# Kernel tuning notes

Hardware: AMD Instinct MI355X
Metric: run time of the kernel (lower is better)

The kernel has to match this reference:

```python
import jax, jax.numpy as jnp
import numpy as np

HEAD_DIM = 64
N_HEADS = 64
N_KV = 8
Q_MULT = N_HEADS // N_KV  # 8
HIDDEN = 2880
SEQ = 1024
BATCH = 2
SLIDING_WINDOW = 128  # layer_idx=0 -> window active
ROPE_THETA = 150000.0
SCALING = 32.0
NTK_ALPHA = 1.0
NTK_BETA = 32.0
INIT_CTX = 4096
EPS = 1e-5


def _rope_caches(seq_len):
    # YaRN rotary caches (static numpy precompute, as in the source module)
    steps = np.arange(0, HEAD_DIM, 2, dtype=np.float32)
    freq = np.power(np.float32(ROPE_THETA), steps / np.float32(HEAD_DIM))
    concentration = np.float32(0.1) * np.log(np.float32(SCALING)) + 1.0
    d_half = np.float32(HEAD_DIM / 2.0)
    log_base = np.log(np.float32(ROPE_THETA))
    low = d_half * np.log(np.float32(INIT_CTX) / (np.float32(NTK_BETA) * np.float32(2.0 * np.pi))) / log_base
    high = d_half * np.log(np.float32(INIT_CTX) / (np.float32(NTK_ALPHA) * np.float32(2.0 * np.pi))) / log_base
    ramp = (np.arange(HEAD_DIM // 2, dtype=np.float32) - low) / (high - low)
    mask = 1.0 - np.clip(ramp, 0.0, 1.0)
    inv_freq = (1.0 / (np.float32(SCALING) * freq)) * (1.0 - mask) + (1.0 / freq) * mask
    pos = np.arange(seq_len, dtype=np.float32)
    freqs = np.einsum('i,j->ij', pos, inv_freq.astype(np.float32))
    cos = (np.cos(freqs) * concentration).astype(np.float32)
    sin = (np.sin(freqs) * concentration).astype(np.float32)
    return jnp.asarray(cos), jnp.asarray(sin)


def _apply_rotary(t, cos, sin):
    # t: (B, S, ..., head_dim); cos/sin: (S, head_dim//2). Rotate-half style.
    shape = (1, t.shape[1]) + (1,) * (t.ndim - 3) + (cos.shape[-1],)
    c = cos.reshape(shape)
    s = sin.reshape(shape)
    first, second = jnp.split(t, 2, axis=-1)
    return jnp.concatenate([first * c - second * s, second * c + first * s], axis=-1)


def setup_inputs() -> dict:
    key = jax.random.key(0)
    ks = jax.random.split(key, 6)
    qkv_dim = (N_HEADS + 2 * N_KV) * HEAD_DIM  # 5120
    return {
        'x': jax.random.normal(ks[0], (BATCH, SEQ, HIDDEN), dtype=jnp.float32),
        'norm_w': jnp.ones((HIDDEN,), dtype=jnp.float32),
        'qkv_w': jax.random.normal(ks[1], (qkv_dim, HIDDEN), dtype=jnp.float32) * 0.02,
        'qkv_b': jax.random.normal(ks[2], (qkv_dim,), dtype=jnp.float32) * 0.02,
        'out_w': jax.random.normal(ks[3], (HIDDEN, N_HEADS * HEAD_DIM), dtype=jnp.float32) * 0.02,
        'out_b': jax.random.normal(ks[4], (HIDDEN,), dtype=jnp.float32) * 0.02,
        'sinks': jax.random.normal(ks[5], (N_HEADS,), dtype=jnp.float32),
    }


def reference(x, norm_w, qkv_w, qkv_b, out_w, out_b, sinks):
    B, S, _ = x.shape
    # RMSNorm (fp32 accumulation)
    xf = x.astype(jnp.float32)
    rms = jnp.mean(xf * xf, axis=-1, keepdims=True)
    t = (xf * jax.lax.rsqrt(rms + EPS) * norm_w).astype(x.dtype)
    # QKV projection (fp32 accumulation)
    qkv = jnp.matmul(t.astype(jnp.float32), qkv_w.T) + qkv_b
    q_dim = N_HEADS * HEAD_DIM
    kv_dim = N_KV * HEAD_DIM
    q = qkv[..., :q_dim].reshape(B, S, N_KV, Q_MULT, HEAD_DIM)
    k = qkv[..., q_dim:q_dim + kv_dim].reshape(B, S, N_KV, HEAD_DIM)
    v = qkv[..., q_dim + kv_dim:].reshape(B, S, N_KV, HEAD_DIM)
    # YaRN rotary embedding
    cos, sin = _rope_caches(S)
    q = _apply_rotary(q, cos, sin)
    k = _apply_rotary(k, cos, sin)
    # causal + sliding-window mask
    neg_inf = jnp.float32(-jnp.inf)
    mask = jnp.triu(jnp.full((S, S), neg_inf, dtype=jnp.float32), k=1)
    mask = mask + jnp.tril(jnp.full((S, S), neg_inf, dtype=jnp.float32), k=-SLIDING_WINDOW)
    sm_scale = jnp.float32(1.0 / np.sqrt(HEAD_DIM))
    # GQA attention with sink logits
    logits = jnp.einsum('bqhmd,bkhd->bhmqk', q, k) * sm_scale + mask[None, None, None]
    sink = jnp.broadcast_to(sinks.reshape(1, N_KV, Q_MULT, 1, 1), (B, N_KV, Q_MULT, S, 1))
    logits = jnp.concatenate([logits, sink], axis=-1)
    w = jax.nn.softmax(logits, axis=-1)[..., :-1]  # drop sink column
    attn = jnp.einsum('bhmqk,bkhd->bqhmd', w, v).reshape(B, S, N_HEADS * HEAD_DIM)
    # output projection (fp32 accumulation) + residual
    out = jnp.matmul(attn, out_w.T) + out_b
    return x + out
```

## Files before the change

kernel.cpp:

```cpp
#include <hip/hip_runtime.h>

typedef unsigned short ushort_t;
typedef __attribute__((ext_vector_type(8))) short short8;
typedef __attribute__((ext_vector_type(8))) __bf16 bf16x8;
typedef __attribute__((ext_vector_type(4))) float float4v;
typedef __attribute__((ext_vector_type(4))) unsigned int uint4v;

__device__ __forceinline__ float bf2f(ushort_t u) {
    unsigned int v = ((unsigned int)u) << 16;
    return __builtin_bit_cast(float, v);
}
__device__ __forceinline__ ushort_t f2bf(float f) {
    unsigned int u = __builtin_bit_cast(unsigned int, f);
    unsigned int lsb = (u >> 16) & 1u;
    u += 0x7fffu + lsb;
    return (ushort_t)(u >> 16);
}
__device__ __forceinline__ uint4v pack8(const ushort_t* r) {
    uint4v u;
#pragma unroll
    for (int i = 0; i < 4; ++i)
        u[i] = (unsigned int)r[2 * i] | ((unsigned int)r[2 * i + 1] << 16);
    return u;
}
__device__ __forceinline__ void unpack8(uint4v u, float* f) {
#pragma unroll
    for (int i = 0; i < 4; ++i) {
        unsigned int x = u[i];
        f[2 * i] = __builtin_bit_cast(float, x << 16);
        f[2 * i + 1] = __builtin_bit_cast(float, x & 0xffff0000u);
    }
}
__device__ __forceinline__ uint4v ld8f32_bf(const float* p) {
    float4v a = *(const float4v*)p;
    float4v b = *(const float4v*)(p + 4);
    ushort_t r[8];
#pragma unroll
    for (int j = 0; j < 4; ++j) { r[j] = f2bf(a[j]); r[4 + j] = f2bf(b[j]); }
    return pack8(r);
}

#if __has_builtin(__builtin_amdgcn_global_load_lds)
#define HAVE_GLDS 1
__device__ __forceinline__ void glds16(const ushort_t* gp, ushort_t* lp) {
    __builtin_amdgcn_global_load_lds((const __attribute__((address_space(1))) void*)gp,
                                     (__attribute__((address_space(3))) void*)lp, 16, 0, 0);
}
#else
#define HAVE_GLDS 0
#endif

template <typename V>
__device__ __forceinline__ auto mfma_sel(V a, V b, float4v c, int)
    -> decltype(__builtin_amdgcn_mfma_f32_16x16x32_bf16(a, b, c, 0, 0, 0)) {
    return __builtin_amdgcn_mfma_f32_16x16x32_bf16(a, b, c, 0, 0, 0);
}
template <typename V>
__device__ __forceinline__ float4v mfma_sel(V a, V b, float4v c, long) {
    return __builtin_amdgcn_mfma_f32_16x16x32_bf16(__builtin_bit_cast(bf16x8, a),
                                                   __builtin_bit_cast(bf16x8, b), c, 0, 0, 0);
}
__device__ __forceinline__ float4v mfma_bf16(short8 a, short8 b, float4v c) {
    return mfma_sel(a, b, c, 0);
}

__device__ __forceinline__ float wave_sum(float v) {
#pragma unroll
    for (int o = 32; o; o >>= 1) v += __shfl_xor(v, o);
    return v;
}

#define HIDDEN 2880
#define NTOK 2048
#define QKV_DIM 5120
#define ATTN_DIM 4096
#define SM_SCALE 0.125f

__global__ __launch_bounds__(256) void f32_to_bf16_dual_kernel(const float* __restrict__ a,
                                                               ushort_t* __restrict__ ao, int na8,
                                                               const float* __restrict__ b,
                                                               ushort_t* __restrict__ bo, int nb8) {
    int idx = blockIdx.x * 256 + threadIdx.x;
    if (idx < na8) {
        *(uint4v*)(ao + (size_t)idx * 8) = ld8f32_bf(a + (size_t)idx * 8);
    } else {
        int j = idx - na8;
        if (j < nb8) *(uint4v*)(bo + (size_t)j * 8) = ld8f32_bf(b + (size_t)j * 8);
    }
}

__global__ __launch_bounds__(256) void rmsnorm_kernel(const float* __restrict__ x,
                                                      const float* __restrict__ wgt,
                                                      ushort_t* __restrict__ out) {
    const int tok = blockIdx.x, tid = threadIdx.x;
    const float* xr = x + (size_t)tok * HIDDEN;
    float v[16];
    float ss = 0.f;
#pragma unroll
    for (int i = 0; i < 2; ++i) {
        int c = tid + i * 256;
        if (c < 360) {
            float4v a = *(const float4v*)(xr + c * 8);
            float4v b = *(const float4v*)(xr + c * 8 + 4);
#pragma unroll
            for (int j = 0; j < 4; ++j) { v[i * 8 + j] = a[j]; v[i * 8 + 4 + j] = b[j]; }
#pragma unroll
            for (int j = 0; j < 8; ++j) ss += v[i * 8 + j] * v[i * 8 + j];
        }
    }
    ss = wave_sum(ss);
    __shared__ float red[4];
    if ((tid & 63) == 0) red[tid >> 6] = ss;
    __syncthreads();
    float scale = rsqrtf((red[0] + red[1] + red[2] + red[3]) * (1.f / 2880.f) + 1e-5f);
#pragma unroll
    for (int i = 0; i < 2; ++i) {
        int c = tid + i * 256;
        if (c < 360) {
            float4v wa = *(const float4v*)(wgt + c * 8);
            float4v wb = *(const float4v*)(wgt + c * 8 + 4);
            ushort_t r[8];
#pragma unroll
            for (int j = 0; j < 4; ++j) {
                r[j] = f2bf(v[i * 8 + j] * scale * wa[j]);
                r[4 + j] = f2bf(v[i * 8 + 4 + j] * scale * wb[j]);
            }
            *(uint4v*)(out + (size_t)tok * HIDDEN + c * 8) = pack8(r);
        }
    }
}

__global__ __launch_bounds__(256) void rope_apply_kernel(ushort_t* __restrict__ qkv) {
    int idx = blockIdx.x * 256 + threadIdx.x;
    int tok = idx / 288;
    int rem = idx - tok * 288;
    int h = rem >> 2, dg = rem & 3;
    int s = tok & 1023;
    size_t base = (size_t)tok * QKV_DIM + (h < 64 ? h * 64 : 4096 + (h - 64) * 64) + dg * 8;
    uint4v u1 = *(const uint4v*)(qkv + base);
    uint4v u2 = *(const uint4v*)(qkv + base + 32);
    float f1[8], f2[8];
    unpack8(u1, f1);
    unpack8(u2, f2);
    const float step = (float)(11.918390573078392 / 32.0);
    const float conc = (float)(1.3465735902799727);
    const float low = (float)(8.092890725542669);
    const float invden = (float)(1.0 / 9.305804387286162);
    ushort_t r1[8], r2[8];
#pragma unroll
    for (int jj = 0; jj < 8; ++jj) {
        int j = dg * 8 + jj;
        float invf = __expf(-(float)j * step);
        float ramp = ((float)j - low) * invden;
        float mask = 1.f - fminf(fmaxf(ramp, 0.f), 1.f);
        float inv_freq = invf * ((1.f - mask) * 0.03125f + mask);
        float ang = (float)s * inv_freq;
        float c = cosf(ang) * conc;
        float sn = sinf(ang) * conc;
        r1[jj] = f2bf(f1[jj] * c - f2[jj] * sn);
        r2[jj] = f2bf(f2[jj] * c + f1[jj] * sn);
    }
    *(uint4v*)(qkv + base) = pack8(r1);
    *(uint4v*)(qkv + base + 32) = pack8(r2);
}

template <int BN, bool RESID, bool OUTF32, bool BF16B>
__global__ __launch_bounds__(256) void gemm_kernel(const ushort_t* __restrict__ A,
                                                   const void* __restrict__ B,
                                                   const float* __restrict__ bias,
                                                   const float* __restrict__ resid,
                                                   void* __restrict__ Cout, int M, int N, int K) {
    constexpr int BM = 128, BK = 64;
    constexpr bool GL = BF16B && (HAVE_GLDS != 0);
    constexpr int LDT = GL ? 64 : 72;
    constexpr int NBUF = GL ? 2 : 1;
    static_assert(BN == 160 || BN == 128 || BN == 96 || BN == 64, "");
    __shared__ __align__(16) ushort_t As[NBUF][BM * LDT];
    __shared__ __align__(16) ushort_t Bs[NBUF][BN * LDT];

    const int m0 = blockIdx.y * BM;
    const int n0 = blockIdx.x * BN;
    const int tid = threadIdx.x;
    const int w = tid >> 6, lane = tid & 63;
    const int quad = lane >> 4, l16 = lane & 15;

    constexpr int WN = BN / 2;
    constexpr int NI = WN / 16;
    const int wm = (w >> 1) * 64;
    const int wn = (w & 1) * WN;

    float4v acc[4][NI];
#pragma unroll
    for (int i = 0; i < 4; ++i)
#pragma unroll
        for (int j = 0; j < NI; ++j) acc[i][j] = (float4v){0.f, 0.f, 0.f, 0.f};

    const int nk = K / BK;

#if HAVE_GLDS
    if constexpr (GL) {
        constexpr int NAI = BM / 32;
        constexpr int NBI = BN / 32;
        const ushort_t* Bp = (const ushort_t*)B;
        const ushort_t* agp[NAI];
        const ushort_t* bgp[NBI];
        ushort_t* alp[2][NAI];
        ushort_t* blp[2][NBI];
#pragma unroll
        for (int i = 0; i < NAI; ++i) {
            int sb = (w * NAI + i) * 64;
            int s = sb + lane, r = s >> 3, p = s & 7, c = p ^ (r & 7);
            agp[i] = A + (size_t)(m0 + r) * K + c * 8;
            alp[0][i] = &As[0][sb * 8];
            alp[1][i] = &As[1][sb * 8];
        }
#pragma unroll
        for (int i = 0; i < NBI; ++i) {
            int sb = (w * NBI + i) * 64;
            int s = sb + lane, r = s >> 3, p = s & 7, c = p ^ (r & 7);
            bgp[i] = Bp + (size_t)(n0 + r) * K + c * 8;
            blp[0][i] = &Bs[0][sb * 8];
            blp[1][i] = &Bs[1][sb * 8];
        }
#pragma unroll
        for (int i = 0; i < NAI; ++i) glds16(agp[i], alp[0][i]);
#pragma unroll
        for (int i = 0; i < NBI; ++i) glds16(bgp[i], blp[0][i]);
        __syncthreads();

        for (int kt = 0; kt < nk; ++kt) {
            const int cur = kt & 1;
            if (kt + 1 < nk) {
                const int k0 = (kt + 1) * BK;
#pragma unroll
                for (int i = 0; i < NAI; ++i) glds16(agp[i] + k0, alp[cur ^ 1][i]);
#pragma unroll
                for (int i = 0; i < NBI; ++i) glds16(bgp[i] + k0, blp[cur ^ 1][i]);
            }
            const ushort_t* Asb = As[cur];
            const ushort_t* Bsb = Bs[cur];
#pragma unroll
            for (int ks = 0; ks < 2; ++ks) {
                short8 af[4], bfr[NI];
#pragma unroll
                for (int mi = 0; mi < 4; ++mi) {
                    int row = wm + mi * 16 + l16;
                    af[mi] = *(const short8*)(Asb + row * LDT + ((ks * 4 + quad) ^ (row & 7)) * 8);
                }
#pragma unroll
                for (int ni = 0; ni < NI; ++ni) {
                    int row = wn + ni * 16 + l16;
                    bfr[ni] = *(const short8*)(Bsb + row * LDT + ((ks * 4 + quad) ^ (row & 7)) * 8);
                }
#pragma unroll
                for (int mi = 0; mi < 4; ++mi)
#pragma unroll
                    for (int ni = 0; ni < NI; ++ni)
                        acc[mi][ni] = mfma_bf16(af[mi], bfr[ni], acc[mi][ni]);
            }
            __syncthreads();
        }
    } else
#endif
    {
        constexpr int ACH = BM * BK / 8 / 256;
        constexpr int BCH = BN * BK / 8 / 256;
        uint4v areg[ACH], breg[BCH];
#pragma unroll
        for (int i = 0; i < ACH; ++i) {
            int c = tid + i * 256, r = c >> 3, col = c & 7;
            areg[i] = *(const uint4v*)(A + (size_t)(m0 + r) * K + col * 8);
        }
#pragma unroll
        for (int i = 0; i < BCH; ++i) {
            int c = tid + i * 256, r = c >> 3, col = c & 7;
            if constexpr (BF16B)
                breg[i] = *(const uint4v*)((const ushort_t*)B + (size_t)(n0 + r) * K + col * 8);
            else
                breg[i] = ld8f32_bf((const float*)B + (size_t)(n0 + r) * K + col * 8);
        }
        for (int kt = 0; kt < nk; ++kt) {
            __syncthreads();
#pragma unroll
            for (int i = 0; i < ACH; ++i) {
                int c = tid + i * 256, r = c >> 3, col = c & 7;
                *(uint4v*)(&As[0][r * LDT + col * 8]) = areg[i];
            }
#pragma unroll
            for (int i = 0; i < BCH; ++i) {
                int c = tid + i * 256, r = c >> 3, col = c & 7;
                *(uint4v*)(&Bs[0][r * LDT + col * 8]) = breg[i];
            }
            __syncthreads();
            if (kt + 1 < nk) {
                const int k0 = (kt + 1) * BK;
#pragma unroll
                for (int i = 0; i < ACH; ++i) {
                    int c = tid + i * 256, r = c >> 3, col = c & 7;
                    areg[i] = *(const uint4v*)(A + (size_t)(m0 + r) * K + k0 + col * 8);
                }
#pragma unroll
                for (int i = 0; i < BCH; ++i) {
                    int c = tid + i * 256, r = c >> 3, col = c & 7;
                    if constexpr (BF16B)
                        breg[i] = *(const uint4v*)((const ushort_t*)B + (size_t)(n0 + r) * K + k0 + col * 8);
                    else
                        breg[i] = ld8f32_bf((const float*)B + (size_t)(n0 + r) * K + k0 + col * 8);
                }
            }
#pragma unroll
            for (int ks = 0; ks < 2; ++ks) {
                short8 af[4], bfr[NI];
#pragma unroll
                for (int mi = 0; mi < 4; ++mi)
                    af[mi] = *(const short8*)(&As[0][(wm + mi * 16 + l16) * LDT + ks * 32 + quad * 8]);
#pragma unroll
                for (int ni = 0; ni < NI; ++ni)
                    bfr[ni] = *(const short8*)(&Bs[0][(wn + ni * 16 + l16) * LDT + ks * 32 + quad * 8]);
#pragma unroll
                for (int mi = 0; mi < 4; ++mi)
#pragma unroll
                    for (int ni = 0; ni < NI; ++ni)
                        acc[mi][ni] = mfma_bf16(af[mi], bfr[ni], acc[mi][ni]);
            }
        }
    }

#pragma unroll
    for (int ni = 0; ni < NI; ++ni) {
        int gc = n0 + wn + ni * 16 + l16;
        float bv = bias[gc];
#pragma unroll
        for (int mi = 0; mi < 4; ++mi) {
#pragma unroll
            for (int r = 0; r < 4; ++r) {
                int gr = m0 + wm + mi * 16 + quad * 4 + r;
                float vv = acc[mi][ni][r] + bv;
                if constexpr (RESID) vv += resid[(size_t)gr * N + gc];
                if constexpr (OUTF32) ((float*)Cout)[(size_t)gr * N + gc] = vv;
                else ((ushort_t*)Cout)[(size_t)gr * N + gc] = f2bf(vv);
            }
        }
    }
}

__global__ __launch_bounds__(256, 2) void attn_mfma_kernel(const ushort_t* __restrict__ qkv,
                                                           const float* __restrict__ sinks,
                                                           ushort_t* __restrict__ attnbuf) {
    constexpr int LDK = 72, LDV = 200, LDP = 200;
    __shared__ __align__(16) ushort_t Ks[192 * LDK];
    __shared__ __align__(16) ushort_t Vt[64 * LDV];
    __shared__ __align__(16) ushort_t Pb[4][16 * LDP];

    const int qc = blockIdx.x, kvh = blockIdx.y >> 1, half = blockIdx.y & 1, b = blockIdx.z;
    const int tid = threadIdx.x;
    const int w = tid >> 6, lane = tid & 63;
    const int quad = lane >> 4, l16 = lane & 15;
    const int w0 = qc * 64 - 127;

    for (int c = tid; c < 192 * 8; c += 256) {
        int row = c >> 3, col8 = c & 7;
        int pos = w0 + row;
        pos = pos < 0 ? 0 : (pos > 1023 ? 1023 : pos);
        size_t gk = ((size_t)(b * 1024 + pos)) * QKV_DIM + 4096 + kvh * 64 + col8 * 8;
        *(uint4v*)(Ks + row * LDK + col8 * 8) = *(const uint4v*)(qkv + gk);
        uint4v vv = *(const uint4v*)(qkv + gk + 512);
        ushort_t vs[8];
#pragma unroll
        for (int i = 0; i < 4; ++i) {
            vs[2 * i] = (ushort_t)(vv[i] & 0xffffu);
            vs[2 * i + 1] = (ushort_t)(vv[i] >> 16);
        }
#pragma unroll
        for (int j = 0; j < 8; ++j) Vt[(col8 * 8 + j) * LDV + row] = vs[j];
    }
    __syncthreads();

    short8 Vf[6][4];
#pragma unroll
    for (int kt = 0; kt < 6; ++kt)
#pragma unroll
        for (int nv = 0; nv < 4; ++nv)
            Vf[kt][nv] = *(const short8*)(Vt + (nv * 16 + l16) * LDV + kt * 32 + quad * 8);

    ushort_t* Pw = Pb[w];
    const int h = kvh * 8 + half * 4 + w;
    const float sink_f = sinks[h];

    for (int qtile = 0; qtile < 4; ++qtile) {
        const int tokb = b * 1024 + qc * 64 + qtile * 16;

        short8 qf[2];
        {
            const ushort_t* qp = qkv + ((size_t)(tokb + l16)) * QKV_DIM + h * 64 + quad * 8;
            qf[0] = *(const short8*)qp;
            qf[1] = *(const short8*)(qp + 32);
        }

        float4v acc[12];
#pragma unroll
        for (int nt = 0; nt < 12; ++nt) acc[nt] = (float4v){0.f, 0.f, 0.f, 0.f};
#pragma unroll
        for (int nt = 0; nt < 12; ++nt) {
#pragma unroll
            for (int ks = 0; ks < 2; ++ks) {
                short8 kf = *(const short8*)(Ks + (nt * 16 + l16) * LDK + ks * 32 + quad * 8);
                acc[nt] = mfma_bf16(qf[ks], kf, acc[nt]);
            }
        }

        float linv[4];
#pragma unroll
        for (int r = 0; r < 4; ++r) {
            const int ql = qtile * 16 + quad * 4 + r;
            float e[12];
            float mx = -1e30f;
#pragma unroll
            for (int nt = 0; nt < 12; ++nt) {
                int row_k = nt * 16 + l16;
                bool valid = (row_k >= ql) && (row_k <= ql + 127) && (w0 + row_k >= 0);
                float s = valid ? acc[nt][r] * SM_SCALE : -1e30f;
                e[nt] = s;
                mx = fmaxf(mx, s);
            }
#pragma unroll
            for (int o = 1; o < 16; o <<= 1) mx = fmaxf(mx, __shfl_xor(mx, o));
            float M = fmaxf(mx, sink_f);
            float ls = 0.f;
#pragma unroll
            for (int nt = 0; nt < 12; ++nt) {
                float ev = (e[nt] > -1e29f) ? __expf(e[nt] - M) : 0.f;
                e[nt] = ev;
                ls += ev;
            }
#pragma unroll
            for (int o = 1; o < 16; o <<= 1) ls += __shfl_xor(ls, o);
            linv[r] = 1.f / (ls + __expf(sink_f - M));
#pragma unroll
            for (int nt = 0; nt < 12; ++nt)
                Pw[(quad * 4 + r) * LDP + nt * 16 + l16] = f2bf(e[nt]);
        }

        float4v accO[4];
#pragma unroll
        for (int nv = 0; nv < 4; ++nv) accO[nv] = (float4v){0.f, 0.f, 0.f, 0.f};
#pragma unroll
        for (int kt = 0; kt < 6; ++kt) {
            short8 pf = *(const short8*)(Pw + l16 * LDP + kt * 32 + quad * 8);
#pragma unroll
            for (int nv = 0; nv < 4; ++nv) accO[nv] = mfma_bf16(pf, Vf[kt][nv], accO[nv]);
        }

#pragma unroll
        for (int r = 0; r < 4; ++r) {
            size_t ob = ((size_t)(tokb + quad * 4 + r)) * ATTN_DIM + h * 64 + l16;
#pragma unroll
            for (int nv = 0; nv < 4; ++nv)
                attnbuf[ob + nv * 16] = f2bf(accO[nv][r] * linv[r]);
        }
    }
}

extern "C" void kernel_launch(void* const* d_in, const int* in_sizes, int n_in,
                              void* d_out, int out_size, void* d_ws, size_t ws_size,
                              hipStream_t stream) {
    const float* x = (const float*)d_in[0];
    const float* norm_w = (const float*)d_in[1];
    const float* qkv_w = (const float*)d_in[2];
    const float* qkv_b = (const float*)d_in[3];
    const float* out_w = (const float*)d_in[4];
    const float* out_b = (const float*)d_in[5];
    const float* sinks = (const float*)d_in[6];
    float* outp = (float*)d_out;
    char* ws = (char*)d_ws;

    if (ws_size >= 86000000ull) {
        ushort_t* qkvbuf = (ushort_t*)ws;
        ushort_t* qkv_w_bf = (ushort_t*)(ws + 20971520);
        ushort_t* attnbuf = (ushort_t*)(ws + 20971520);
        ushort_t* Tbuf = (ushort_t*)(ws + 50462720);
        ushort_t* out_w_bf = (ushort_t*)(ws + 62259200);

        f32_to_bf16_dual_kernel<<<12960, 256, 0, stream>>>(qkv_w, qkv_w_bf, 1843200,
                                                           out_w, out_w_bf, 1474560);
        rmsnorm_kernel<<<NTOK, 256, 0, stream>>>(x, norm_w, Tbuf);
        gemm_kernel<160, false, false, true><<<dim3(32, 16), 256, 0, stream>>>(
            Tbuf, qkv_w_bf, qkv_b, nullptr, qkvbuf, NTOK, QKV_DIM, HIDDEN);
        rope_apply_kernel<<<2304, 256, 0, stream>>>(qkvbuf);
        attn_mfma_kernel<<<dim3(16, 16, 2), 256, 0, stream>>>(qkvbuf, sinks, attnbuf);
        gemm_kernel<96, true, true, true><<<dim3(30, 16), 256, 0, stream>>>(
            attnbuf, out_w_bf, out_b, x, outp, NTOK, HIDDEN, ATTN_DIM);
    } else {
        ushort_t* qkvbuf = (ushort_t*)ws;
        ushort_t* attnbuf = (ushort_t*)(ws + 20971520);
        ushort_t* Tbuf = (ushort_t*)d_out;

        rmsnorm_kernel<<<NTOK, 256, 0, stream>>>(x, norm_w, Tbuf);
        gemm_kernel<128, false, false, false><<<dim3(40, 16), 256, 0, stream>>>(
            Tbuf, qkv_w, qkv_b, nullptr, qkvbuf, NTOK, QKV_DIM, HIDDEN);
        rope_apply_kernel<<<2304, 256, 0, stream>>>(qkvbuf);
        attn_mfma_kernel<<<dim3(16, 16, 2), 256, 0, stream>>>(qkvbuf, sinks, attnbuf);
        gemm_kernel<96, true, true, false><<<dim3(30, 16), 256, 0, stream>>>(
            attnbuf, out_w, out_b, x, outp, NTOK, HIDDEN, ATTN_DIM);
    }
}
```

Baseline: 323.1 us.

## Deepen GEMM global-to-LDS prefetch with manual vmcnt waits and swizzle workgroup order

```diff
diff --git a/kernel.cpp b/kernel.cpp
--- a/kernel.cpp
+++ b/kernel.cpp
@@ -178,8 +178,15 @@
     __shared__ __align__(16) ushort_t As[NBUF][BM * LDT];
     __shared__ __align__(16) ushort_t Bs[NBUF][BN * LDT];
 
-    const int m0 = blockIdx.y * BM;
-    const int n0 = blockIdx.x * BN;
+    const int nbx = gridDim.x;
+    int wg = blockIdx.y * nbx + blockIdx.x;
+    {
+        const int nwg = nbx * gridDim.y;
+        const int cpx = nwg >> 3;
+        wg = (wg & 7) * cpx + (wg >> 3);
+    }
+    const int m0 = (wg / nbx) * BM;
+    const int n0 = (wg % nbx) * BN;
     const int tid = threadIdx.x;
     const int w = tid >> 6, lane = tid & 63;
     const int quad = lane >> 4, l16 = lane & 15;
@@ -201,6 +208,7 @@
     if constexpr (GL) {
         constexpr int NAI = BM / 32;
         constexpr int NBI = BN / 32;
+        constexpr int L = NAI + NBI;
         const ushort_t* Bp = (const ushort_t*)B;
         const ushort_t* agp[NAI];
         const ushort_t* bgp[NBI];
@@ -226,17 +234,21 @@
         for (int i = 0; i < NAI; ++i) glds16(agp[i], alp[0][i]);
 #pragma unroll
         for (int i = 0; i < NBI; ++i) glds16(bgp[i], blp[0][i]);
-        __syncthreads();
+        if (nk > 1) {
+#pragma unroll
+            for (int i = 0; i < NAI; ++i) glds16(agp[i] + BK, alp[1][i]);
+#pragma unroll
+            for (int i = 0; i < NBI; ++i) glds16(bgp[i] + BK, blp[1][i]);
+        }
 
         for (int kt = 0; kt < nk; ++kt) {
             const int cur = kt & 1;
-            if (kt + 1 < nk) {
-                const int k0 = (kt + 1) * BK;
-#pragma unroll
-                for (int i = 0; i < NAI; ++i) glds16(agp[i] + k0, alp[cur ^ 1][i]);
-#pragma unroll
-                for (int i = 0; i < NBI; ++i) glds16(bgp[i] + k0, blp[cur ^ 1][i]);
-            }
+            if (kt + 1 < nk)
+                asm volatile("s_waitcnt vmcnt(%0)" ::"n"(L) : "memory");
+            else
+                asm volatile("s_waitcnt vmcnt(0)" ::: "memory");
+            __builtin_amdgcn_s_barrier();
+            asm volatile("" ::: "memory");
             const ushort_t* Asb = As[cur];
             const ushort_t* Bsb = Bs[cur];
 #pragma unroll
@@ -258,7 +270,16 @@
                     for (int ni = 0; ni < NI; ++ni)
                         acc[mi][ni] = mfma_bf16(af[mi], bfr[ni], acc[mi][ni]);
             }
-            __syncthreads();
+            asm volatile("s_waitcnt lgkmcnt(0)" ::: "memory");
+            __builtin_amdgcn_s_barrier();
+            asm volatile("" ::: "memory");
+            if (kt + 2 < nk) {
+                const int k0 = (kt + 2) * BK;
+#pragma unroll
+                for (int i = 0; i < NAI; ++i) glds16(agp[i] + k0, alp[cur][i]);
+#pragma unroll
+                for (int i = 0; i < NBI; ++i) glds16(bgp[i] + k0, blp[cur][i]);
+            }
         }
     } else
 #endif
```

New measurement: 339.7 us. +5.2%, slower.
